# Performance work log

Measured on AMD Instinct MI355X. Metric: run time of the kernel, lower is better.

Reference implementation:

```python
import jax, jax.numpy as jnp
import numpy as np

N_NODES, N_PARENTS, K_WORDS, MAX_DEG = 16384, 8192, 32, 4
VOCAB, HID, NCLASS = 100000, 64, 4
NEG_INF = -1e30


def setup_inputs() -> dict:
    key = jax.random.key(0)
    ks = jax.random.split(key, 16)
    L = N_NODES - N_PARENTS
    # tree: leaves-first node ordering; parent i is node L+i, children are earlier nodes
    rng = np.random.default_rng(0)
    tree = np.full((N_PARENTS, MAX_DEG + 1), -1, dtype=np.int32)
    for i in range(N_PARENTS):
        hi = L + i
        nc = int(rng.integers(1, MAX_DEG + 1))
        ch = rng.choice(hi, size=min(nc, hi), replace=False)
        tree[i, :len(ch)] = ch
        tree[i, MAX_DEG] = hi  # parent slot, ignored (row[:-1] used)
    s = 0.1
    return {
        "x_word": jax.random.uniform(ks[0], (N_NODES, K_WORDS), jnp.float32),
        "x_index": jax.random.randint(ks[1], (N_NODES, K_WORDS), 0, VOCAB, jnp.int32),
        "tree": jnp.asarray(tree),
        "E_bu": s * jax.random.normal(ks[2], (HID, VOCAB), jnp.float32),
        "W_z_bu": s * jax.random.normal(ks[3], (HID, HID), jnp.float32),
        "U_z_bu": s * jax.random.normal(ks[4], (HID, HID), jnp.float32),
        "b_z_bu": jnp.zeros((1, HID), jnp.float32),
        "W_r_bu": s * jax.random.normal(ks[5], (HID, HID), jnp.float32),
        "U_r_bu": s * jax.random.normal(ks[6], (HID, HID), jnp.float32),
        "b_r_bu": jnp.zeros((1, HID), jnp.float32),
        "W_h_bu": s * jax.random.normal(ks[7], (HID, HID), jnp.float32),
        "U_h_bu": s * jax.random.normal(ks[8], (HID, HID), jnp.float32),
        "b_h_bu": jnp.zeros((1, HID), jnp.float32),
        "W_attn": s * jax.random.normal(ks[9], (HID, HID), jnp.float32),
        "W_out_bu": s * jax.random.normal(ks[10], (NCLASS, HID), jnp.float32),
        "b_out_bu": jnp.zeros((NCLASS,), jnp.float32),
    }


def reference(x_word, x_index, tree, E_bu, W_z_bu, U_z_bu, b_z_bu,
              W_r_bu, U_r_bu, b_r_bu, W_h_bu, U_h_bu, b_h_bu,
              W_attn, W_out_bu, b_out_bu):
    N = x_word.shape[0]
    P = tree.shape[0]
    L = N - P  # leaves first
    H = E_bu.shape[0]
    # node embedding xe[n] = x_word[n] @ E_bu[:, x_index[n]].T  -> [N,H]
    Eg = E_bu.T[x_index]                       # [N,K,H] gather (memory-bound)
    xe = jnp.einsum('nk,nkh->nh', x_word, Eg)  # [N,H]
    # Leaf update: child_h = zeros -> attn uniform, h_tilde = 0
    z_l = jax.nn.sigmoid(xe[:L] @ W_z_bu.T + b_z_bu)
    c_l = jnp.tanh(xe[:L] @ W_h_bu.T + b_h_bu)
    leaf_h = (1.0 - z_l) * c_l                 # z*0 + (1-z)*c
    node_h0 = jnp.zeros((N, H), xe.dtype).at[:L].set(leaf_h)
    children = tree[:, :-1]                    # [P, D] child indices, -1 padded

    def step(node_h, inp):
        idx, ch = inp
        mask = ch > -1
        ci = jnp.where(mask, ch, 0)
        child_h = node_h[ci]                   # [D,H]
        pxe = xe[L + idx]                      # [H]
        # attn = softmax(sigmoid(parent_xe @ W_attn @ child_h.T)) over valid children
        logits = jax.nn.sigmoid(pxe @ (W_attn @ child_h.T))
        attn = jax.nn.softmax(jnp.where(mask, logits, NEG_INF))
        h_tilde = attn @ child_h               # [H]  (LayerNorm output discarded in original)
        z = jax.nn.sigmoid(pxe @ W_z_bu.T + h_tilde @ U_z_bu.T + b_z_bu[0])
        r = jax.nn.sigmoid(pxe @ W_r_bu.T + h_tilde @ U_r_bu.T + b_r_bu[0])
        c = jnp.tanh(pxe @ W_h_bu.T + (r * h_tilde) @ U_h_bu.T + b_h_bu[0])
        h = z * h_tilde + (1.0 - z) * c        # dropout in eval = identity
        return node_h.at[L + idx].set(h), None

    node_h, _ = jax.lax.scan(step, node_h0, (jnp.arange(P), children))
    final = jnp.max(node_h[L:], axis=0)        # [H]
    return jax.nn.softmax((W_out_bu * final).sum(axis=1) + b_out_bu)
```

## Files before the change

kernel.cpp:

```cpp
#include <hip/hip_runtime.h>
#include <math.h>

#define NN 16384
#define NP 8192
#define NL 8192
#define KW 32
#define VC 100000
#define SENT  0xFFFFFFFFu
#define NEVER 0xFFFFFFFEu
#define CLEAN_EPOCH 1000

__device__ __forceinline__ float sigmoidf_(float x){ return 1.0f/(1.0f+expf(-x)); }

__global__ void __launch_bounds__(256) k_setup(const float* __restrict__ E, float* __restrict__ ET,
    const float* __restrict__ Wz, const float* __restrict__ Wr, const float* __restrict__ Wh,
    const float* __restrict__ Uz, const float* __restrict__ Ur, const float* __restrict__ Uh,
    float* __restrict__ WT, float* __restrict__ node_h, int* done, int* g_rem, int et_blocks){
  __shared__ float tile[64][65];
  int b = blockIdx.x;
  int lane = threadIdx.x & 63, ty = threadIdx.x >> 6;
  if (b < et_blocks){
    int v0 = b*64;
    for (int h = ty; h < 64; h += 4){
      int v = v0 + lane;
      tile[h][lane] = (v < VC) ? E[(size_t)h*VC + v] : 0.f;
    }
    __syncthreads();
    for (int vv = ty; vv < 64; vv += 4){
      int v = v0 + vv;
      if (v < VC) ET[v*64 + lane] = tile[lane][vv];
    }
  } else if (b < et_blocks + 6){
    int m = b - et_blocks;
    const float* src = (m==0)?Wz:(m==1)?Wr:(m==2)?Wh:(m==3)?Uz:(m==4)?Ur:Uh;
    float* dst = WT + m*4096;
    for (int h = ty; h < 64; h += 4) tile[h][lane] = src[h*64 + lane];
    __syncthreads();
    for (int k = ty; k < 64; k += 4) dst[k*64 + lane] = tile[lane][k];
  } else if (b < et_blocks + 6 + 4096){
    size_t idx = (size_t)(b - et_blocks - 6)*256 + threadIdx.x;
    ((unsigned int*)node_h)[idx] = SENT;
  } else {
    int idx = (b - et_blocks - 6 - 4096)*256 + threadIdx.x;
    if (idx < NP) done[idx] = 0;
    if (idx == 0) *g_rem = NP;
  }
}

__device__ __forceinline__ float gru_compute(int lane,
    int c0,int c1,int c2,int c3,
    float chv0,float chv1,float chv2,float chv3,
    float q, float pzv, float prv, float pcv,
    const float* __restrict__ UzT, const float* __restrict__ UrT,
    const float* __restrict__ UhT)
{
  float d0=q*chv0, d1=q*chv1, d2=q*chv2, d3=q*chv3;
  #pragma unroll
  for (int off=32; off; off>>=1){
    d0 += __shfl_xor(d0, off); d1 += __shfl_xor(d1, off);
    d2 += __shfl_xor(d2, off); d3 += __shfl_xor(d3, off);
  }
  float l0 = (c0>=0)? sigmoidf_(d0) : -1e30f;
  float l1 = (c1>=0)? sigmoidf_(d1) : -1e30f;
  float l2 = (c2>=0)? sigmoidf_(d2) : -1e30f;
  float l3 = (c3>=0)? sigmoidf_(d3) : -1e30f;
  float mx = fmaxf(fmaxf(l0,l1), fmaxf(l2,l3));
  float e0=expf(l0-mx), e1=expf(l1-mx), e2=expf(l2-mx), e3=expf(l3-mx);
  float inv = 1.f/(e0+e1+e2+e3);
  float ht = (e0*chv0 + e1*chv1 + e2*chv2 + e3*chv3)*inv;
  float az0=0.f, az1=0.f, ar0=0.f, ar1=0.f;
  #pragma unroll 8
  for (int k=0;k<64;k+=2){
    float h0 = __shfl(ht, k), h1 = __shfl(ht, k+1);
    az0 += h0 * UzT[k*64+lane];     az1 += h1 * UzT[(k+1)*64+lane];
    ar0 += h0 * UrT[k*64+lane];     ar1 += h1 * UrT[(k+1)*64+lane];
  }
  float z = sigmoidf_(pzv + az0+az1);
  float r = sigmoidf_(prv + ar0+ar1);
  float rh = r*ht;
  float ac0=0.f, ac1=0.f, ac2=0.f, ac3=0.f;
  #pragma unroll 8
  for (int k=0;k<64;k+=4){
    float r0 = __shfl(rh, k),   r1 = __shfl(rh, k+1);
    float r2 = __shfl(rh, k+2), r3 = __shfl(rh, k+3);
    ac0 += r0 * UhT[k*64+lane];     ac1 += r1 * UhT[(k+1)*64+lane];
    ac2 += r2 * UhT[(k+2)*64+lane]; ac3 += r3 * UhT[(k+3)*64+lane];
  }
  float cc = tanhf(pcv + (ac0+ac1)+(ac2+ac3));
  return z*ht + (1.f-z)*cc;
}

__device__ __forceinline__ void fused_body(int wid, int lane, float xev,
    const float* __restrict__ WzT, const float* __restrict__ WrT,
    const float* __restrict__ WhT, const float* __restrict__ Wa,
    const float* __restrict__ bz, const float* __restrict__ br,
    const float* __restrict__ bh,
    const float* __restrict__ UzT, const float* __restrict__ UrT,
    const float* __restrict__ UhT, const int* __restrict__ tree,
    float* node_h, float* pz, float* pr, float* pc, float* qa,
    int* done, int* g_rem)
{
  unsigned int* nhu = (unsigned int*)node_h;
  if (wid < NL){
    float az0=0.f, az1=0.f, ah0=0.f, ah1=0.f;
    #pragma unroll 8
    for (int k=0;k<64;k+=2){
      float x0 = __shfl(xev, k), x1 = __shfl(xev, k+1);
      az0 += x0 * WzT[k*64+lane];     az1 += x1 * WzT[(k+1)*64+lane];
      ah0 += x0 * WhT[k*64+lane];     ah1 += x1 * WhT[(k+1)*64+lane];
    }
    float z = sigmoidf_(az0+az1 + bz[lane]);
    float c = tanhf(ah0+ah1 + bh[lane]);
    float h = (1.f-z)*c;
    atomicExch(&nhu[(size_t)wid*64 + lane], __float_as_uint(h));
    return;
  }
  int i = wid - NL;
  float az=0.f, ar=0.f, ah=0.f, aq=0.f;
  #pragma unroll 4
  for (int k=0;k<64;++k){
    float xk = __shfl(xev, k);
    az += xk * WzT[k*64+lane];
    ar += xk * WrT[k*64+lane];
    ah += xk * WhT[k*64+lane];
    aq += xk * Wa [k*64+lane];
  }
  float pzv = az + bz[lane], prv = ar + br[lane], pcv = ah + bh[lane], q = aq;
  pz[i*64+lane] = pzv; pr[i*64+lane] = prv; pc[i*64+lane] = pcv; qa[i*64+lane] = q;
  const int* tr = tree + i*5;
  int c0=tr[0], c1=tr[1], c2=tr[2], c3=tr[3];
  unsigned int u0 = (c0>=0)? nhu[(size_t)c0*64+lane] : 0u;
  unsigned int u1 = (c1>=0)? nhu[(size_t)c1*64+lane] : 0u;
  unsigned int u2 = (c2>=0)? nhu[(size_t)c2*64+lane] : 0u;
  unsigned int u3 = (c3>=0)? nhu[(size_t)c3*64+lane] : 0u;
  bool p0 = __any((int)(u0==SENT)), p1 = __any((int)(u1==SENT));
  bool p2 = __any((int)(u2==SENT)), p3 = __any((int)(u3==SENT));
  int rounds = 0;
  while ((p0|p1|p2|p3) && rounds < (1<<16)){
    if (p0){ if (u0==SENT) u0 = atomicCAS(&nhu[(size_t)c0*64+lane], NEVER, NEVER); p0 = __any((int)(u0==SENT)); }
    if (p1){ if (u1==SENT) u1 = atomicCAS(&nhu[(size_t)c1*64+lane], NEVER, NEVER); p1 = __any((int)(u1==SENT)); }
    if (p2){ if (u2==SENT) u2 = atomicCAS(&nhu[(size_t)c2*64+lane], NEVER, NEVER); p2 = __any((int)(u2==SENT)); }
    if (p3){ if (u3==SENT) u3 = atomicCAS(&nhu[(size_t)c3*64+lane], NEVER, NEVER); p3 = __any((int)(u3==SENT)); }
    if (p0|p1|p2|p3){ __builtin_amdgcn_s_sleep(4); ++rounds; }
  }
  if (p0|p1|p2|p3) return;
  float h = gru_compute(lane, c0,c1,c2,c3,
                        __uint_as_float(u0), __uint_as_float(u1),
                        __uint_as_float(u2), __uint_as_float(u3),
                        q, pzv, prv, pcv, UzT, UrT, UhT);
  atomicExch(&nhu[(size_t)(NL+i)*64 + lane], __float_as_uint(h));
  if (lane==0){ done[i] = 1; atomicAdd(g_rem, -1); }
}

__global__ void __launch_bounds__(256) k_fused(const float* __restrict__ xw,
    const int* __restrict__ xi, const float* __restrict__ ET,
    const float* __restrict__ WzT, const float* __restrict__ WrT,
    const float* __restrict__ WhT, const float* __restrict__ Wa,
    const float* __restrict__ bz, const float* __restrict__ br,
    const float* __restrict__ bh,
    const float* __restrict__ UzT, const float* __restrict__ UrT,
    const float* __restrict__ UhT, const int* __restrict__ tree,
    float* node_h, float* pz, float* pr, float* pc, float* qa,
    int* done, int* g_rem)
{
  int wid = blockIdx.x*4 + (threadIdx.x>>6);
  int lane = threadIdx.x & 63;
  if (wid >= NN) return;
  int   idxl = (lane < KW) ? xi[wid*KW + lane] : 0;
  float wl   = (lane < KW) ? xw[wid*KW + lane] : 0.f;
  float xev = 0.f;
  #pragma unroll 8
  for (int k = 0; k < KW; ++k){
    int   vk = __shfl(idxl, k);
    float wk = __shfl(wl,   k);
    xev += wk * ET[vk*64 + lane];
  }
  fused_body(wid, lane, xev, WzT,WrT,WhT,Wa, bz,br,bh, UzT,UrT,UhT, tree,
             node_h, pz,pr,pc,qa, done, g_rem);
}

__global__ void __launch_bounds__(256) k_fused_direct(const float* __restrict__ xw,
    const int* __restrict__ xi, const float* __restrict__ E,
    const float* __restrict__ WzT, const float* __restrict__ WrT,
    const float* __restrict__ WhT, const float* __restrict__ Wa,
    const float* __restrict__ bz, const float* __restrict__ br,
    const float* __restrict__ bh,
    const float* __restrict__ UzT, const float* __restrict__ UrT,
    const float* __restrict__ UhT, const int* __restrict__ tree,
    float* node_h, float* pz, float* pr, float* pc, float* qa,
    int* done, int* g_rem)
{
  int wid = blockIdx.x*4 + (threadIdx.x>>6);
  int lane = threadIdx.x & 63;
  if (wid >= NN) return;
  const float* w = xw + wid*KW;
  const int*   v = xi + wid*KW;
  const float* Erow = E + (size_t)lane*VC;
  float xev = 0.f;
  for (int k = 0; k < KW; ++k) xev += w[k] * Erow[v[k]];
  fused_body(wid, lane, xev, WzT,WrT,WhT,Wa, bz,br,bh, UzT,UrT,UhT, tree,
             node_h, pz,pr,pc,qa, done, g_rem);
}

__device__ __forceinline__ bool lvl_ready(int c, int lvl, const int* done){
  if (c < NL) return true;
  int e = done[c - NL];
  return (e > 0 && e < lvl);
}

__global__ void __launch_bounds__(256) k_cleanup(const int* __restrict__ tree,
    const float* __restrict__ qa, const float* __restrict__ pz,
    const float* __restrict__ pr, const float* __restrict__ pc,
    const float* __restrict__ UzT, const float* __restrict__ UrT,
    const float* __restrict__ UhT,
    float* node_h, int* done, int* g_rem)
{
  int rem = *g_rem;
  if (rem <= 0) return;
  __shared__ int cnt_s;
  int w = threadIdx.x >> 6, lane = threadIdx.x & 63;
  int epoch = CLEAN_EPOCH;
  while (rem > 0){
    if (threadIdx.x == 0) cnt_s = 0;
    __syncthreads();
    int my = 0;
    for (int i = w; i < NP; i += 4){
      if (done[i]) continue;
      const int* tr = tree + i*5;
      int c0=tr[0], c1=tr[1], c2=tr[2], c3=tr[3];
      if (!(lvl_ready(c0,epoch,done) && lvl_ready(c1,epoch,done)
         && lvl_ready(c2,epoch,done) && lvl_ready(c3,epoch,done))) continue;
      float chv0 = (c0>=0)? node_h[c0*64+lane] : 0.f;
      float chv1 = (c1>=0)? node_h[c1*64+lane] : 0.f;
      float chv2 = (c2>=0)? node_h[c2*64+lane] : 0.f;
      float chv3 = (c3>=0)? node_h[c3*64+lane] : 0.f;
      float h = gru_compute(lane, c0,c1,c2,c3, chv0,chv1,chv2,chv3,
                            qa[i*64+lane], pz[i*64+lane], pr[i*64+lane], pc[i*64+lane],
                            UzT, UrT, UhT);
      node_h[(size_t)(NL+i)*64+lane] = h;
      if (lane==0) done[i] = epoch;
      ++my;
    }
    if (lane==0 && my) atomicAdd(&cnt_s, my);
    __syncthreads();
    rem -= cnt_s;
    ++epoch;
    __syncthreads();
  }
}

__global__ void k_max1(const float* __restrict__ node_h, float* __restrict__ partial){
  __shared__ float sm[4][64];
  int lane = threadIdx.x & 63, w = threadIdx.x>>6;
  int base = NL + blockIdx.x*128;
  float m = -1e30f;
  for (int r = w; r < 128; r += 4)
    m = fmaxf(m, node_h[(size_t)(base+r)*64 + lane]);
  sm[w][lane] = m;
  __syncthreads();
  if (w==0){
    m = fmaxf(fmaxf(sm[0][lane],sm[1][lane]), fmaxf(sm[2][lane],sm[3][lane]));
    partial[blockIdx.x*64+lane] = m;
  }
}

__global__ void k_max2(const float* __restrict__ partial, const float* __restrict__ Wout,
                       const float* __restrict__ bout, float* __restrict__ out){
  int lane = threadIdx.x;
  float m = -1e30f;
  for (int b=0;b<64;++b) m = fmaxf(m, partial[b*64+lane]);
  float s0 = Wout[0*64+lane]*m;
  float s1 = Wout[1*64+lane]*m;
  float s2 = Wout[2*64+lane]*m;
  float s3 = Wout[3*64+lane]*m;
  #pragma unroll
  for (int off=32; off; off>>=1){
    s0 += __shfl_xor(s0, off);
    s1 += __shfl_xor(s1, off);
    s2 += __shfl_xor(s2, off);
    s3 += __shfl_xor(s3, off);
  }
  s0 += bout[0]; s1 += bout[1]; s2 += bout[2]; s3 += bout[3];
  float mx = fmaxf(fmaxf(s0,s1), fmaxf(s2,s3));
  float e0=expf(s0-mx), e1=expf(s1-mx), e2=expf(s2-mx), e3=expf(s3-mx);
  float inv = 1.f/(e0+e1+e2+e3);
  if (lane==0){
    out[0]=e0*inv; out[1]=e1*inv; out[2]=e2*inv; out[3]=e3*inv;
  }
}

__global__ void k_ws_sentinel(float* out, float wsmb){
  if (threadIdx.x < 4) out[threadIdx.x] = wsmb;
}

extern "C" void kernel_launch(void* const* d_in, const int* in_sizes, int n_in,
                              void* d_out, int out_size, void* d_ws, size_t ws_size,
                              hipStream_t stream){
  const float* x_word = (const float*)d_in[0];
  const int*   x_index= (const int*)d_in[1];
  const int*   tree   = (const int*)d_in[2];
  const float* E      = (const float*)d_in[3];
  const float* Wz     = (const float*)d_in[4];
  const float* Uz     = (const float*)d_in[5];
  const float* bz     = (const float*)d_in[6];
  const float* Wr     = (const float*)d_in[7];
  const float* Ur     = (const float*)d_in[8];
  const float* br     = (const float*)d_in[9];
  const float* Wh     = (const float*)d_in[10];
  const float* Uh     = (const float*)d_in[11];
  const float* bh     = (const float*)d_in[12];
  const float* Wa     = (const float*)d_in[13];
  const float* Wout   = (const float*)d_in[14];
  const float* bout   = (const float*)d_in[15];
  float* out = (float*)d_out;

  float* ws = (float*)d_ws;

  const size_t R0_FULL = 6400000;
  const size_t R0_FB   = 4096;
  const size_t TAIL    = 2097152 + 1048576 + 24576 + NP + 1;
  const size_t FULL_NEED = (R0_FULL + TAIL) * 4;
  const size_t FB_NEED   = (R0_FB   + TAIL) * 4;

  bool full = (ws_size >= FULL_NEED);
  bool fb   = (!full && ws_size >= FB_NEED);
  if (!full && !fb){
    k_ws_sentinel<<<1, 64, 0, stream>>>(out, (float)(ws_size >> 20));
    return;
  }

  float* ET   = ws;
  float* part = ws;
  size_t r0   = full ? R0_FULL : R0_FB;
  float* qa    = ws + r0;
  float* pz    = qa + 524288;
  float* pr    = pz + 524288;
  float* pc    = pr + 524288;
  float* nodeh = pc + 524288;
  float* WT    = nodeh + 1048576;
  int*   done  = (int*)(WT + 24576);
  int*   g_rem = done + NP;
  float* WzT = WT,       *WrT = WT+4096,  *WhT = WT+8192;
  float* UzT = WT+12288, *UrT = WT+16384, *UhT = WT+20480;

  int et_blocks = full ? (VC+63)/64 : 0;
  k_setup<<<et_blocks + 6 + 4096 + NP/256, 256, 0, stream>>>(
      E, ET, Wz, Wr, Wh, Uz, Ur, Uh, WT, nodeh, done, g_rem, et_blocks);
  if (full)
    k_fused<<<NN/4, 256, 0, stream>>>(x_word, x_index, ET, WzT, WrT, WhT, Wa,
                                      bz, br, bh, UzT, UrT, UhT, tree,
                                      nodeh, pz, pr, pc, qa, done, g_rem);
  else
    k_fused_direct<<<NN/4, 256, 0, stream>>>(x_word, x_index, E, WzT, WrT, WhT, Wa,
                                             bz, br, bh, UzT, UrT, UhT, tree,
                                             nodeh, pz, pr, pc, qa, done, g_rem);
  k_cleanup<<<1,  256, 0, stream>>>(tree, qa, pz, pr, pc, UzT, UrT, UhT,
                                    nodeh, done, g_rem);
  k_max1   <<<64, 256, 0, stream>>>(nodeh, part);
  k_max2   <<<1,   64, 0, stream>>>(part, Wout, bout, out);
}
```

Measured before the change: 164.1 us.

## Replace spin-wait parent scheduling with dependency-counted work handoff and fused max

```diff
diff --git a/kernel.cpp b/kernel.cpp
--- a/kernel.cpp
+++ b/kernel.cpp
@@ -6,16 +6,27 @@
 #define NL 8192
 #define KW 32
 #define VC 100000
+#define REVW 8
 #define SENT  0xFFFFFFFFu
 #define NEVER 0xFFFFFFFEu
-#define CLEAN_EPOCH 1000
+#define UMAP_NEGINF 0x007FFFFFu
 
 __device__ __forceinline__ float sigmoidf_(float x){ return 1.0f/(1.0f+expf(-x)); }
+__device__ __forceinline__ unsigned int umap(float f){
+  unsigned int b = __float_as_uint(f);
+  return (b & 0x80000000u) ? ~b : (b | 0x80000000u);
+}
+__device__ __forceinline__ float uunmap(unsigned int u){
+  unsigned int b = (u & 0x80000000u) ? (u & 0x7FFFFFFFu) : ~u;
+  return __uint_as_float(b);
+}
 
 __global__ void __launch_bounds__(256) k_setup(const float* __restrict__ E, float* __restrict__ ET,
     const float* __restrict__ Wz, const float* __restrict__ Wr, const float* __restrict__ Wh,
     const float* __restrict__ Uz, const float* __restrict__ Ur, const float* __restrict__ Uh,
-    float* __restrict__ WT, float* __restrict__ node_h, int* done, int* g_rem, int et_blocks){
+    float* __restrict__ WT, unsigned int* node_h, unsigned int* pact,
+    const int* __restrict__ tree, int* pending, int* rcnt, int* rev,
+    int* g_rem, unsigned int* gmax, int et_blocks){
   __shared__ float tile[64][65];
   int b = blockIdx.x;
   int lane = threadIdx.x & 63, ty = threadIdx.x >> 6;
@@ -39,11 +50,29 @@
     for (int k = ty; k < 64; k += 4) dst[k*64 + lane] = tile[lane][k];
   } else if (b < et_blocks + 6 + 4096){
     size_t idx = (size_t)(b - et_blocks - 6)*256 + threadIdx.x;
-    ((unsigned int*)node_h)[idx] = SENT;
+    node_h[idx] = SENT;
+  } else if (b < et_blocks + 6 + 4096 + 8192){
+    size_t idx = (size_t)(b - et_blocks - 6 - 4096)*256 + threadIdx.x;
+    pact[idx] = SENT;
   } else {
-    int idx = (b - et_blocks - 6 - 4096)*256 + threadIdx.x;
-    if (idx < NP) done[idx] = 0;
+    int idx = (b - et_blocks - 6 - 4096 - 8192)*256 + threadIdx.x;
+    if (idx < NP){
+      const int* tr = tree + idx*5;
+      int cnt = 0;
+      #pragma unroll
+      for (int j=0;j<4;++j){
+        int c = tr[j];
+        if (c >= NL){
+          ++cnt;
+          int cc = c - NL;
+          int slot = atomicAdd(&rcnt[cc], 1);
+          if (slot < REVW) rev[cc*REVW + slot] = idx;
+        }
+      }
+      pending[idx] = cnt + 1;
+    }
     if (idx == 0) *g_rem = NP;
+    if (idx < 512) gmax[idx] = UMAP_NEGINF;
   }
 }
 
@@ -90,17 +119,26 @@
   return z*ht + (1.f-z)*cc;
 }
 
-__device__ __forceinline__ void fused_body(int wid, int lane, float xev,
+__device__ __forceinline__ unsigned int read_sync(unsigned int* p, int* budget){
+  unsigned int u = *p;
+  while (__any((int)(u == SENT)) && *budget > 0){
+    if (u == SENT) u = atomicCAS(p, NEVER, NEVER);
+    if (__any((int)(u == SENT))){ __builtin_amdgcn_s_sleep(2); --*budget; }
+  }
+  return u;
+}
+
+__device__ __forceinline__ void fused_body(int wid, int w, int lane, float xev,
     const float* __restrict__ WzT, const float* __restrict__ WrT,
     const float* __restrict__ WhT, const float* __restrict__ Wa,
     const float* __restrict__ bz, const float* __restrict__ br,
     const float* __restrict__ bh,
     const float* __restrict__ UzT, const float* __restrict__ UrT,
     const float* __restrict__ UhT, const int* __restrict__ tree,
-    float* node_h, float* pz, float* pr, float* pc, float* qa,
-    int* done, int* g_rem)
+    unsigned int* nhu, unsigned int* pact, int* pending,
+    const int* __restrict__ rcnt, const int* __restrict__ rev,
+    int* g_rem, unsigned int* gmax, int* stk)
 {
-  unsigned int* nhu = (unsigned int*)node_h;
   if (wid < NL){
     float az0=0.f, az1=0.f, ah0=0.f, ah1=0.f;
     #pragma unroll 8
@@ -111,8 +149,7 @@
     }
     float z = sigmoidf_(az0+az1 + bz[lane]);
     float c = tanhf(ah0+ah1 + bh[lane]);
-    float h = (1.f-z)*c;
-    atomicExch(&nhu[(size_t)wid*64 + lane], __float_as_uint(h));
+    atomicExch(&nhu[(size_t)wid*64 + lane], __float_as_uint((1.f-z)*c));
     return;
   }
   int i = wid - NL;
@@ -125,31 +162,62 @@
     ah += xk * WhT[k*64+lane];
     aq += xk * Wa [k*64+lane];
   }
-  float pzv = az + bz[lane], prv = ar + br[lane], pcv = ah + bh[lane], q = aq;
-  pz[i*64+lane] = pzv; pr[i*64+lane] = prv; pc[i*64+lane] = pcv; qa[i*64+lane] = q;
-  const int* tr = tree + i*5;
-  int c0=tr[0], c1=tr[1], c2=tr[2], c3=tr[3];
-  unsigned int u0 = (c0>=0)? nhu[(size_t)c0*64+lane] : 0u;
-  unsigned int u1 = (c1>=0)? nhu[(size_t)c1*64+lane] : 0u;
-  unsigned int u2 = (c2>=0)? nhu[(size_t)c2*64+lane] : 0u;
-  unsigned int u3 = (c3>=0)? nhu[(size_t)c3*64+lane] : 0u;
-  bool p0 = __any((int)(u0==SENT)), p1 = __any((int)(u1==SENT));
-  bool p2 = __any((int)(u2==SENT)), p3 = __any((int)(u3==SENT));
-  int rounds = 0;
-  while ((p0|p1|p2|p3) && rounds < (1<<16)){
-    if (p0){ if (u0==SENT) u0 = atomicCAS(&nhu[(size_t)c0*64+lane], NEVER, NEVER); p0 = __any((int)(u0==SENT)); }
-    if (p1){ if (u1==SENT) u1 = atomicCAS(&nhu[(size_t)c1*64+lane], NEVER, NEVER); p1 = __any((int)(u1==SENT)); }
-    if (p2){ if (u2==SENT) u2 = atomicCAS(&nhu[(size_t)c2*64+lane], NEVER, NEVER); p2 = __any((int)(u2==SENT)); }
-    if (p3){ if (u3==SENT) u3 = atomicCAS(&nhu[(size_t)c3*64+lane], NEVER, NEVER); p3 = __any((int)(u3==SENT)); }
-    if (p0|p1|p2|p3){ __builtin_amdgcn_s_sleep(4); ++rounds; }
-  }
-  if (p0|p1|p2|p3) return;
-  float h = gru_compute(lane, c0,c1,c2,c3,
-                        __uint_as_float(u0), __uint_as_float(u1),
-                        __uint_as_float(u2), __uint_as_float(u3),
-                        q, pzv, prv, pcv, UzT, UrT, UhT);
-  atomicExch(&nhu[(size_t)(NL+i)*64 + lane], __float_as_uint(h));
-  if (lane==0){ done[i] = 1; atomicAdd(g_rem, -1); }
+  float q0 = aq, pz0 = az + bz[lane], pr0 = ar + br[lane], pc0 = ah + bh[lane];
+  unsigned int* pa = pact + (size_t)i*256;
+  atomicExch(&pa[0*64+lane], __float_as_uint(q0));
+  atomicExch(&pa[1*64+lane], __float_as_uint(pz0));
+  atomicExch(&pa[2*64+lane], __float_as_uint(pc0));
+  atomicExch(&pa[3*64+lane], __float_as_uint(pr0));
+  int nn = -1, sp = 0;
+  if (lane == 0){
+    if (atomicSub(&pending[i], 1) == 1) nn = i;
+  }
+  int next = __shfl(nn, 0);
+  bool ownregs = true;
+  while (next >= 0){
+    int cur = next;
+    int budget = 1<<16;
+    float q, pzv, prv, pcv;
+    if (ownregs && cur == i){ q=q0; pzv=pz0; prv=pr0; pcv=pc0; }
+    else {
+      unsigned int* pb = pact + (size_t)cur*256;
+      q   = __uint_as_float(read_sync(&pb[0*64+lane], &budget));
+      pzv = __uint_as_float(read_sync(&pb[1*64+lane], &budget));
+      pcv = __uint_as_float(read_sync(&pb[2*64+lane], &budget));
+      prv = __uint_as_float(read_sync(&pb[3*64+lane], &budget));
+    }
+    const int* tr = tree + cur*5;
+    int c0=tr[0], c1=tr[1], c2=tr[2], c3=tr[3];
+    unsigned int u0 = (c0>=0)? read_sync(&nhu[(size_t)c0*64+lane], &budget) : 0u;
+    unsigned int u1 = (c1>=0)? read_sync(&nhu[(size_t)c1*64+lane], &budget) : 0u;
+    unsigned int u2 = (c2>=0)? read_sync(&nhu[(size_t)c2*64+lane], &budget) : 0u;
+    unsigned int u3 = (c3>=0)? read_sync(&nhu[(size_t)c3*64+lane], &budget) : 0u;
+    bool bad = __any((int)(u0==SENT)) || __any((int)(u1==SENT)) ||
+               __any((int)(u2==SENT)) || __any((int)(u3==SENT));
+    nn = -1;
+    if (!bad){
+      float h = gru_compute(lane, c0,c1,c2,c3,
+                            __uint_as_float(u0), __uint_as_float(u1),
+                            __uint_as_float(u2), __uint_as_float(u3),
+                            q, pzv, prv, pcv, UzT, UrT, UhT);
+      atomicExch(&nhu[(size_t)(NL+cur)*64 + lane], __float_as_uint(h));
+      atomicMax(&gmax[(cur&7)*64 + lane], umap(h));
+      if (lane == 0){
+        atomicAdd(g_rem, -1);
+        int rc = rcnt[cur]; if (rc > REVW) rc = REVW;
+        for (int j = 0; j < rc; ++j){
+          int cons = rev[cur*REVW + j];
+          if (atomicSub(&pending[cons], 1) == 1){
+            if (nn < 0) nn = cons;
+            else if (sp < 12) stk[sp++] = cons;
+          }
+        }
+      }
+    }
+    if (lane == 0 && nn < 0 && sp > 0) nn = stk[--sp];
+    next = __shfl(nn, 0);
+    ownregs = false;
+  }
 }
 
 __global__ void __launch_bounds__(256) k_fused(const float* __restrict__ xw,
@@ -160,11 +228,13 @@
     const float* __restrict__ bh,
     const float* __restrict__ UzT, const float* __restrict__ UrT,
     const float* __restrict__ UhT, const int* __restrict__ tree,
-    float* node_h, float* pz, float* pr, float* pc, float* qa,
-    int* done, int* g_rem)
+    unsigned int* nhu, unsigned int* pact, int* pending,
+    const int* __restrict__ rcnt, const int* __restrict__ rev,
+    int* g_rem, unsigned int* gmax)
 {
-  int wid = blockIdx.x*4 + (threadIdx.x>>6);
-  int lane = threadIdx.x & 63;
+  __shared__ int stk_s[4][12];
+  int w = threadIdx.x >> 6, lane = threadIdx.x & 63;
+  int wid = blockIdx.x*4 + w;
   if (wid >= NN) return;
   int   idxl = (lane < KW) ? xi[wid*KW + lane] : 0;
   float wl   = (lane < KW) ? xw[wid*KW + lane] : 0.f;
@@ -175,8 +245,8 @@
     float wk = __shfl(wl,   k);
     xev += wk * ET[vk*64 + lane];
   }
-  fused_body(wid, lane, xev, WzT,WrT,WhT,Wa, bz,br,bh, UzT,UrT,UhT, tree,
-             node_h, pz,pr,pc,qa, done, g_rem);
+  fused_body(wid, w, lane, xev, WzT,WrT,WhT,Wa, bz,br,bh, UzT,UrT,UhT, tree,
+             nhu, pact, pending, rcnt, rev, g_rem, gmax, stk_s[w]);
 }
 
 __global__ void __launch_bounds__(256) k_fused_direct(const float* __restrict__ xw,
@@ -187,105 +257,89 @@
     const float* __restrict__ bh,
     const float* __restrict__ UzT, const float* __restrict__ UrT,
     const float* __restrict__ UhT, const int* __restrict__ tree,
-    float* node_h, float* pz, float* pr, float* pc, float* qa,
-    int* done, int* g_rem)
+    unsigned int* nhu, unsigned int* pact, int* pending,
+    const int* __restrict__ rcnt, const int* __restrict__ rev,
+    int* g_rem, unsigned int* gmax)
 {
-  int wid = blockIdx.x*4 + (threadIdx.x>>6);
-  int lane = threadIdx.x & 63;
+  __shared__ int stk_s[4][12];
+  int w = threadIdx.x >> 6, lane = threadIdx.x & 63;
+  int wid = blockIdx.x*4 + w;
   if (wid >= NN) return;
-  const float* w = xw + wid*KW;
-  const int*   v = xi + wid*KW;
+  const float* wv = xw + wid*KW;
+  const int*   v  = xi + wid*KW;
   const float* Erow = E + (size_t)lane*VC;
   float xev = 0.f;
-  for (int k = 0; k < KW; ++k) xev += w[k] * Erow[v[k]];
-  fused_body(wid, lane, xev, WzT,WrT,WhT,Wa, bz,br,bh, UzT,UrT,UhT, tree,
-             node_h, pz,pr,pc,qa, done, g_rem);
-}
-
-__device__ __forceinline__ bool lvl_ready(int c, int lvl, const int* done){
-  if (c < NL) return true;
-  int e = done[c - NL];
-  return (e > 0 && e < lvl);
-}
-
-__global__ void __launch_bounds__(256) k_cleanup(const int* __restrict__ tree,
-    const float* __restrict__ qa, const float* __restrict__ pz,
-    const float* __restrict__ pr, const float* __restrict__ pc,
+  for (int k = 0; k < KW; ++k) xev += wv[k] * Erow[v[k]];
+  fused_body(wid, w, lane, xev, WzT,WrT,WhT,Wa, bz,br,bh, UzT,UrT,UhT, tree,
+             nhu, pact, pending, rcnt, rev, g_rem, gmax, stk_s[w]);
+}
+
+__global__ void __launch_bounds__(256) k_finish(const int* __restrict__ tree,
+    const unsigned int* __restrict__ pact,
     const float* __restrict__ UzT, const float* __restrict__ UrT,
     const float* __restrict__ UhT,
-    float* node_h, int* done, int* g_rem)
+    unsigned int* nhu, int* g_rem, unsigned int* gmax,
+    const float* __restrict__ Wout, const float* __restrict__ bout,
+    float* __restrict__ out)
 {
+  __shared__ int cnt_s;
+  __shared__ float sm[64];
+  int w = threadIdx.x >> 6, lane = threadIdx.x & 63;
   int rem = *g_rem;
-  if (rem <= 0) return;
-  __shared__ int cnt_s;
-  int w = threadIdx.x >> 6, lane = threadIdx.x & 63;
-  int epoch = CLEAN_EPOCH;
   while (rem > 0){
     if (threadIdx.x == 0) cnt_s = 0;
     __syncthreads();
     int my = 0;
     for (int i = w; i < NP; i += 4){
-      if (done[i]) continue;
+      if (nhu[(size_t)(NL+i)*64] != SENT) continue;
       const int* tr = tree + i*5;
       int c0=tr[0], c1=tr[1], c2=tr[2], c3=tr[3];
-      if (!(lvl_ready(c0,epoch,done) && lvl_ready(c1,epoch,done)
-         && lvl_ready(c2,epoch,done) && lvl_ready(c3,epoch,done))) continue;
-      float chv0 = (c0>=0)? node_h[c0*64+lane] : 0.f;
-      float chv1 = (c1>=0)? node_h[c1*64+lane] : 0.f;
-      float chv2 = (c2>=0)? node_h[c2*64+lane] : 0.f;
-      float chv3 = (c3>=0)? node_h[c3*64+lane] : 0.f;
+      bool ready = (c0<0 || nhu[(size_t)c0*64] != SENT) &&
+                   (c1<0 || nhu[(size_t)c1*64] != SENT) &&
+                   (c2<0 || nhu[(size_t)c2*64] != SENT) &&
+                   (c3<0 || nhu[(size_t)c3*64] != SENT);
+      if (!ready) continue;
+      float chv0 = (c0>=0)? __uint_as_float(nhu[(size_t)c0*64+lane]) : 0.f;
+      float chv1 = (c1>=0)? __uint_as_float(nhu[(size_t)c1*64+lane]) : 0.f;
+      float chv2 = (c2>=0)? __uint_as_float(nhu[(size_t)c2*64+lane]) : 0.f;
+      float chv3 = (c3>=0)? __uint_as_float(nhu[(size_t)c3*64+lane]) : 0.f;
+      const unsigned int* pb = pact + (size_t)i*256;
+      float q   = __uint_as_float(pb[0*64+lane]);
+      float pzv = __uint_as_float(pb[1*64+lane]);
+      float pcv = __uint_as_float(pb[2*64+lane]);
+      float prv = __uint_as_float(pb[3*64+lane]);
       float h = gru_compute(lane, c0,c1,c2,c3, chv0,chv1,chv2,chv3,
-                            qa[i*64+lane], pz[i*64+lane], pr[i*64+lane], pc[i*64+lane],
-                            UzT, UrT, UhT);
-      node_h[(size_t)(NL+i)*64+lane] = h;
-      if (lane==0) done[i] = epoch;
+                            q, pzv, prv, pcv, UzT, UrT, UhT);
+      nhu[(size_t)(NL+i)*64+lane] = __float_as_uint(h);
+      atomicMax(&gmax[(i&7)*64+lane], umap(h));
       ++my;
     }
     if (lane==0 && my) atomicAdd(&cnt_s, my);
     __syncthreads();
     rem -= cnt_s;
-    ++epoch;
+    if (cnt_s == 0) break;
     __syncthreads();
   }
-}
-
-__global__ void k_max1(const float* __restrict__ node_h, float* __restrict__ partial){
-  __shared__ float sm[4][64];
-  int lane = threadIdx.x & 63, w = threadIdx.x>>6;
-  int base = NL + blockIdx.x*128;
-  float m = -1e30f;
-  for (int r = w; r < 128; r += 4)
-    m = fmaxf(m, node_h[(size_t)(base+r)*64 + lane]);
-  sm[w][lane] = m;
   __syncthreads();
-  if (w==0){
-    m = fmaxf(fmaxf(sm[0][lane],sm[1][lane]), fmaxf(sm[2][lane],sm[3][lane]));
-    partial[blockIdx.x*64+lane] = m;
-  }
-}
-
-__global__ void k_max2(const float* __restrict__ partial, const float* __restrict__ Wout,
-                       const float* __restrict__ bout, float* __restrict__ out){
-  int lane = threadIdx.x;
-  float m = -1e30f;
-  for (int b=0;b<64;++b) m = fmaxf(m, partial[b*64+lane]);
-  float s0 = Wout[0*64+lane]*m;
-  float s1 = Wout[1*64+lane]*m;
-  float s2 = Wout[2*64+lane]*m;
-  float s3 = Wout[3*64+lane]*m;
-  #pragma unroll
-  for (int off=32; off; off>>=1){
-    s0 += __shfl_xor(s0, off);
-    s1 += __shfl_xor(s1, off);
-    s2 += __shfl_xor(s2, off);
-    s3 += __shfl_xor(s3, off);
-  }
-  s0 += bout[0]; s1 += bout[1]; s2 += bout[2]; s3 += bout[3];
-  float mx = fmaxf(fmaxf(s0,s1), fmaxf(s2,s3));
-  float e0=expf(s0-mx), e1=expf(s1-mx), e2=expf(s2-mx), e3=expf(s3-mx);
-  float inv = 1.f/(e0+e1+e2+e3);
-  if (lane==0){
-    out[0]=e0*inv; out[1]=e1*inv; out[2]=e2*inv; out[3]=e3*inv;
+  if (w == 0){
+    float m = -1e30f;
+    #pragma unroll
+    for (int c = 0; c < 8; ++c) m = fmaxf(m, uunmap(gmax[c*64+lane]));
+    sm[lane] = m;
+    float s0 = Wout[0*64+lane]*m, s1 = Wout[1*64+lane]*m;
+    float s2 = Wout[2*64+lane]*m, s3 = Wout[3*64+lane]*m;
+    #pragma unroll
+    for (int off=32; off; off>>=1){
+      s0 += __shfl_xor(s0, off); s1 += __shfl_xor(s1, off);
+      s2 += __shfl_xor(s2, off); s3 += __shfl_xor(s3, off);
+    }
+    s0 += bout[0]; s1 += bout[1]; s2 += bout[2]; s3 += bout[3];
+    float mx = fmaxf(fmaxf(s0,s1), fmaxf(s2,s3));
+    float e0=expf(s0-mx), e1=expf(s1-mx), e2=expf(s2-mx), e3=expf(s3-mx);
+    float inv = 1.f/(e0+e1+e2+e3);
+    if (lane==0){
+      out[0]=e0*inv; out[1]=e1*inv; out[2]=e2*inv; out[3]=e3*inv;
+    }
   }
 }
 
@@ -317,10 +371,9 @@
   float* ws = (float*)d_ws;
 
   const size_t R0_FULL = 6400000;
-  const size_t R0_FB   = 4096;
-  const size_t TAIL    = 2097152 + 1048576 + 24576 + NP + 1;
+  const size_t TAIL = (size_t)2097152 + 1048576 + 24576 + NP + NP + NP*REVW + 1 + 512;
   const size_t FULL_NEED = (R0_FULL + TAIL) * 4;
-  const size_t FB_NEED   = (R0_FB   + TAIL) * 4;
+  const size_t FB_NEED   = TAIL * 4;
 
   bool full = (ws_size >= FULL_NEED);
   bool fb   = (!full && ws_size >= FB_NEED);
@@ -329,33 +382,34 @@
     return;
   }
 
-  float* ET   = ws;
-  float* part = ws;
-  size_t r0   = full ? R0_FULL : R0_FB;
-  float* qa    = ws + r0;
-  float* pz    = qa + 524288;
-  float* pr    = pz + 524288;
-  float* pc    = pr + 524288;
-  float* nodeh = pc + 524288;
-  float* WT    = nodeh + 1048576;
-  int*   done  = (int*)(WT + 24576);
-  int*   g_rem = done + NP;
+  float* ET = ws;
+  size_t r0 = full ? R0_FULL : 0;
+  unsigned int* pact  = (unsigned int*)(ws + r0);
+  unsigned int* nhu   = pact + (size_t)NP*256;
+  float* WT   = (float*)(nhu + (size_t)NN*64);
+  int* pending = (int*)(WT + 24576);
+  int* rcnt    = pending + NP;
+  int* rev     = rcnt + NP;
+  int* g_rem   = rev + NP*REVW;
+  unsigned int* gmax = (unsigned int*)(g_rem + 1);
   float* WzT = WT,       *WrT = WT+4096,  *WhT = WT+8192;
   float* UzT = WT+12288, *UrT = WT+16384, *UhT = WT+20480;
 
+  hipMemsetAsync(rcnt, 0, NP*sizeof(int), stream);
+
   int et_blocks = full ? (VC+63)/64 : 0;
-  k_setup<<<et_blocks + 6 + 4096 + NP/256, 256, 0, stream>>>(
-      E, ET, Wz, Wr, Wh, Uz, Ur, Uh, WT, nodeh, done, g_rem, et_blocks);
+  int nblocks = et_blocks + 6 + 4096 + 8192 + NP/256;
+  k_setup<<<nblocks, 256, 0, stream>>>(E, ET, Wz, Wr, Wh, Uz, Ur, Uh, WT,
+                                       nhu, pact, tree, pending, rcnt, rev,
+                                       g_rem, gmax, et_blocks);
   if (full)
     k_fused<<<NN/4, 256, 0, stream>>>(x_word, x_index, ET, WzT, WrT, WhT, Wa,
                                       bz, br, bh, UzT, UrT, UhT, tree,
-                                      nodeh, pz, pr, pc, qa, done, g_rem);
+                                      nhu, pact, pending, rcnt, rev, g_rem, gmax);
   else
     k_fused_direct<<<NN/4, 256, 0, stream>>>(x_word, x_index, E, WzT, WrT, WhT, Wa,
                                              bz, br, bh, UzT, UrT, UhT, tree,
-                                             nodeh, pz, pr, pc, qa, done, g_rem);
-  k_cleanup<<<1,  256, 0, stream>>>(tree, qa, pz, pr, pc, UzT, UrT, UhT,
-                                    nodeh, done, g_rem);
-  k_max1   <<<64, 256, 0, stream>>>(nodeh, part);
-  k_max2   <<<1,   64, 0, stream>>>(part, Wout, bout, out);
-}
+                                             nhu, pact, pending, rcnt, rev, g_rem, gmax);
+  k_finish<<<1, 256, 0, stream>>>(tree, pact, UzT, UrT, UhT, nhu, g_rem, gmax,
+                                  Wout, bout, out);
+}
```

Measured after the change: 269.6 us. 64.2% more time.

## Use row-level ready flags, fused atomic max, and merged finish kernel

Applied to the files above, without the earlier changes.

```diff
diff --git a/kernel.cpp b/kernel.cpp
--- a/kernel.cpp
+++ b/kernel.cpp
@@ -8,14 +8,23 @@
 #define VC 100000
 #define SENT  0xFFFFFFFFu
 #define NEVER 0xFFFFFFFEu
-#define CLEAN_EPOCH 1000
+#define UMAP_NEGINF 0x007FFFFFu
 
 __device__ __forceinline__ float sigmoidf_(float x){ return 1.0f/(1.0f+expf(-x)); }
+__device__ __forceinline__ unsigned int umap(float f){
+  unsigned int b = __float_as_uint(f);
+  return (b & 0x80000000u) ? ~b : (b | 0x80000000u);
+}
+__device__ __forceinline__ float uunmap(unsigned int u){
+  unsigned int b = (u & 0x80000000u) ? (u & 0x7FFFFFFFu) : ~u;
+  return __uint_as_float(b);
+}
 
 __global__ void __launch_bounds__(256) k_setup(const float* __restrict__ E, float* __restrict__ ET,
     const float* __restrict__ Wz, const float* __restrict__ Wr, const float* __restrict__ Wh,
     const float* __restrict__ Uz, const float* __restrict__ Ur, const float* __restrict__ Uh,
-    float* __restrict__ WT, float* __restrict__ node_h, int* done, int* g_rem, int et_blocks){
+    float* __restrict__ WT, unsigned int* node_h, int* g_rem, unsigned int* gmax,
+    int et_blocks){
   __shared__ float tile[64][65];
   int b = blockIdx.x;
   int lane = threadIdx.x & 63, ty = threadIdx.x >> 6;
@@ -39,12 +48,19 @@
     for (int k = ty; k < 64; k += 4) dst[k*64 + lane] = tile[lane][k];
   } else if (b < et_blocks + 6 + 4096){
     size_t idx = (size_t)(b - et_blocks - 6)*256 + threadIdx.x;
-    ((unsigned int*)node_h)[idx] = SENT;
+    node_h[idx] = SENT;
   } else {
     int idx = (b - et_blocks - 6 - 4096)*256 + threadIdx.x;
-    if (idx < NP) done[idx] = 0;
+    if (idx < 512) gmax[idx] = UMAP_NEGINF;
     if (idx == 0) *g_rem = NP;
   }
+}
+
+__device__ __forceinline__ void publish_row(unsigned int* row, int lane, float h){
+  unsigned int hb = __float_as_uint(h);
+  if (lane) atomicExch(&row[lane], hb);
+  asm volatile("s_waitcnt vmcnt(0)" ::: "memory");
+  if (!lane) atomicExch(&row[0], hb);
 }
 
 __device__ __forceinline__ float gru_compute(int lane,
@@ -97,10 +113,9 @@
     const float* __restrict__ bh,
     const float* __restrict__ UzT, const float* __restrict__ UrT,
     const float* __restrict__ UhT, const int* __restrict__ tree,
-    float* node_h, float* pz, float* pr, float* pc, float* qa,
-    int* done, int* g_rem)
-{
-  unsigned int* nhu = (unsigned int*)node_h;
+    unsigned int* nhu, float* pz, float* pr, float* pc, float* qa,
+    int* g_rem, unsigned int* gmax)
+{
   if (wid < NL){
     float az0=0.f, az1=0.f, ah0=0.f, ah1=0.f;
     #pragma unroll 8
@@ -111,8 +126,7 @@
     }
     float z = sigmoidf_(az0+az1 + bz[lane]);
     float c = tanhf(ah0+ah1 + bh[lane]);
-    float h = (1.f-z)*c;
-    atomicExch(&nhu[(size_t)wid*64 + lane], __float_as_uint(h));
+    publish_row(&nhu[(size_t)wid*64], lane, (1.f-z)*c);
     return;
   }
   int i = wid - NL;
@@ -125,7 +139,7 @@
     ah += xk * WhT[k*64+lane];
     aq += xk * Wa [k*64+lane];
   }
-  float pzv = az + bz[lane], prv = ar + br[lane], pcv = ah + bh[lane], q = aq;
+  float q = aq, pzv = az + bz[lane], prv = ar + br[lane], pcv = ah + bh[lane];
   pz[i*64+lane] = pzv; pr[i*64+lane] = prv; pc[i*64+lane] = pcv; qa[i*64+lane] = q;
   const int* tr = tree + i*5;
   int c0=tr[0], c1=tr[1], c2=tr[2], c3=tr[3];
@@ -133,23 +147,36 @@
   unsigned int u1 = (c1>=0)? nhu[(size_t)c1*64+lane] : 0u;
   unsigned int u2 = (c2>=0)? nhu[(size_t)c2*64+lane] : 0u;
   unsigned int u3 = (c3>=0)? nhu[(size_t)c3*64+lane] : 0u;
-  bool p0 = __any((int)(u0==SENT)), p1 = __any((int)(u1==SENT));
-  bool p2 = __any((int)(u2==SENT)), p3 = __any((int)(u3==SENT));
-  int rounds = 0;
-  while ((p0|p1|p2|p3) && rounds < (1<<16)){
-    if (p0){ if (u0==SENT) u0 = atomicCAS(&nhu[(size_t)c0*64+lane], NEVER, NEVER); p0 = __any((int)(u0==SENT)); }
-    if (p1){ if (u1==SENT) u1 = atomicCAS(&nhu[(size_t)c1*64+lane], NEVER, NEVER); p1 = __any((int)(u1==SENT)); }
-    if (p2){ if (u2==SENT) u2 = atomicCAS(&nhu[(size_t)c2*64+lane], NEVER, NEVER); p2 = __any((int)(u2==SENT)); }
-    if (p3){ if (u3==SENT) u3 = atomicCAS(&nhu[(size_t)c3*64+lane], NEVER, NEVER); p3 = __any((int)(u3==SENT)); }
-    if (p0|p1|p2|p3){ __builtin_amdgcn_s_sleep(4); ++rounds; }
-  }
-  if (p0|p1|p2|p3) return;
+  bool anyS = __any((int)(u0==SENT)) || __any((int)(u1==SENT)) ||
+              __any((int)(u2==SENT)) || __any((int)(u3==SENT));
+  if (anyS){
+    int myc = (lane==0)?c0:(lane==1)?c1:(lane==2)?c2:(lane==3)?c3:-1;
+    bool need = (lane < 4) && (myc >= 0);
+    unsigned int* myp = &nhu[(size_t)(need ? myc : 0)*64];
+    bool rdy = !need;
+    if (need) rdy = (atomicCAS(myp, NEVER, NEVER) != SENT);
+    int rounds = 0;
+    while (!__all((int)rdy)){
+      if (rounds < 4) __builtin_amdgcn_s_sleep(1);
+      else            __builtin_amdgcn_s_sleep(8);
+      if (!rdy) rdy = (atomicCAS(myp, NEVER, NEVER) != SENT);
+      if (++rounds > (1<<14)) break;
+    }
+    if (!__all((int)rdy)) return;
+    if (c0>=0 && u0==SENT) u0 = atomicCAS(&nhu[(size_t)c0*64+lane], NEVER, NEVER);
+    if (c1>=0 && u1==SENT) u1 = atomicCAS(&nhu[(size_t)c1*64+lane], NEVER, NEVER);
+    if (c2>=0 && u2==SENT) u2 = atomicCAS(&nhu[(size_t)c2*64+lane], NEVER, NEVER);
+    if (c3>=0 && u3==SENT) u3 = atomicCAS(&nhu[(size_t)c3*64+lane], NEVER, NEVER);
+    if (__any((int)(u0==SENT)) || __any((int)(u1==SENT)) ||
+        __any((int)(u2==SENT)) || __any((int)(u3==SENT))) return;
+  }
   float h = gru_compute(lane, c0,c1,c2,c3,
                         __uint_as_float(u0), __uint_as_float(u1),
                         __uint_as_float(u2), __uint_as_float(u3),
                         q, pzv, prv, pcv, UzT, UrT, UhT);
-  atomicExch(&nhu[(size_t)(NL+i)*64 + lane], __float_as_uint(h));
-  if (lane==0){ done[i] = 1; atomicAdd(g_rem, -1); }
+  publish_row(&nhu[(size_t)(NL+i)*64], lane, h);
+  atomicMax(&gmax[(i&7)*64 + lane], umap(h));
+  if (lane==0) atomicAdd(g_rem, -1);
 }
 
 __global__ void __launch_bounds__(256) k_fused(const float* __restrict__ xw,
@@ -160,8 +187,8 @@
     const float* __restrict__ bh,
     const float* __restrict__ UzT, const float* __restrict__ UrT,
     const float* __restrict__ UhT, const int* __restrict__ tree,
-    float* node_h, float* pz, float* pr, float* pc, float* qa,
-    int* done, int* g_rem)
+    unsigned int* nhu, float* pz, float* pr, float* pc, float* qa,
+    int* g_rem, unsigned int* gmax)
 {
   int wid = blockIdx.x*4 + (threadIdx.x>>6);
   int lane = threadIdx.x & 63;
@@ -176,7 +203,7 @@
     xev += wk * ET[vk*64 + lane];
   }
   fused_body(wid, lane, xev, WzT,WrT,WhT,Wa, bz,br,bh, UzT,UrT,UhT, tree,
-             node_h, pz,pr,pc,qa, done, g_rem);
+             nhu, pz,pr,pc,qa, g_rem, gmax);
 }
 
 __global__ void __launch_bounds__(256) k_fused_direct(const float* __restrict__ xw,
@@ -187,105 +214,85 @@
     const float* __restrict__ bh,
     const float* __restrict__ UzT, const float* __restrict__ UrT,
     const float* __restrict__ UhT, const int* __restrict__ tree,
-    float* node_h, float* pz, float* pr, float* pc, float* qa,
-    int* done, int* g_rem)
+    unsigned int* nhu, float* pz, float* pr, float* pc, float* qa,
+    int* g_rem, unsigned int* gmax)
 {
   int wid = blockIdx.x*4 + (threadIdx.x>>6);
   int lane = threadIdx.x & 63;
   if (wid >= NN) return;
-  const float* w = xw + wid*KW;
-  const int*   v = xi + wid*KW;
+  const float* wv = xw + wid*KW;
+  const int*   v  = xi + wid*KW;
   const float* Erow = E + (size_t)lane*VC;
   float xev = 0.f;
-  for (int k = 0; k < KW; ++k) xev += w[k] * Erow[v[k]];
+  for (int k = 0; k < KW; ++k) xev += wv[k] * Erow[v[k]];
   fused_body(wid, lane, xev, WzT,WrT,WhT,Wa, bz,br,bh, UzT,UrT,UhT, tree,
-             node_h, pz,pr,pc,qa, done, g_rem);
-}
-
-__device__ __forceinline__ bool lvl_ready(int c, int lvl, const int* done){
-  if (c < NL) return true;
-  int e = done[c - NL];
-  return (e > 0 && e < lvl);
-}
-
-__global__ void __launch_bounds__(256) k_cleanup(const int* __restrict__ tree,
+             nhu, pz,pr,pc,qa, g_rem, gmax);
+}
+
+__global__ void __launch_bounds__(256) k_finish(const int* __restrict__ tree,
     const float* __restrict__ qa, const float* __restrict__ pz,
     const float* __restrict__ pr, const float* __restrict__ pc,
     const float* __restrict__ UzT, const float* __restrict__ UrT,
     const float* __restrict__ UhT,
-    float* node_h, int* done, int* g_rem)
-{
-  int rem = *g_rem;
-  if (rem <= 0) return;
+    unsigned int* nhu, int* g_rem, unsigned int* gmax,
+    const float* __restrict__ Wout, const float* __restrict__ bout,
+    float* __restrict__ out)
+{
   __shared__ int cnt_s;
   int w = threadIdx.x >> 6, lane = threadIdx.x & 63;
-  int epoch = CLEAN_EPOCH;
+  int rem = *g_rem;
   while (rem > 0){
     if (threadIdx.x == 0) cnt_s = 0;
     __syncthreads();
     int my = 0;
     for (int i = w; i < NP; i += 4){
-      if (done[i]) continue;
+      if (nhu[(size_t)(NL+i)*64] != SENT) continue;
       const int* tr = tree + i*5;
       int c0=tr[0], c1=tr[1], c2=tr[2], c3=tr[3];
-      if (!(lvl_ready(c0,epoch,done) && lvl_ready(c1,epoch,done)
-         && lvl_ready(c2,epoch,done) && lvl_ready(c3,epoch,done))) continue;
-      float chv0 = (c0>=0)? node_h[c0*64+lane] : 0.f;
-      float chv1 = (c1>=0)? node_h[c1*64+lane] : 0.f;
-      float chv2 = (c2>=0)? node_h[c2*64+lane] : 0.f;
-      float chv3 = (c3>=0)? node_h[c3*64+lane] : 0.f;
+      bool ready = (c0<0 || nhu[(size_t)c0*64] != SENT) &&
+                   (c1<0 || nhu[(size_t)c1*64] != SENT) &&
+                   (c2<0 || nhu[(size_t)c2*64] != SENT) &&
+                   (c3<0 || nhu[(size_t)c3*64] != SENT);
+      if (!ready) continue;
+      float chv0 = (c0>=0)? __uint_as_float(nhu[(size_t)c0*64+lane]) : 0.f;
+      float chv1 = (c1>=0)? __uint_as_float(nhu[(size_t)c1*64+lane]) : 0.f;
+      float chv2 = (c2>=0)? __uint_as_float(nhu[(size_t)c2*64+lane]) : 0.f;
+      float chv3 = (c3>=0)? __uint_as_float(nhu[(size_t)c3*64+lane]) : 0.f;
       float h = gru_compute(lane, c0,c1,c2,c3, chv0,chv1,chv2,chv3,
                             qa[i*64+lane], pz[i*64+lane], pr[i*64+lane], pc[i*64+lane],
                             UzT, UrT, UhT);
-      node_h[(size_t)(NL+i)*64+lane] = h;
-      if (lane==0) done[i] = epoch;
+      nhu[(size_t)(NL+i)*64+lane] = __float_as_uint(h);
+      atomicMax(&gmax[(i&7)*64+lane], umap(h));
       ++my;
     }
     if (lane==0 && my) atomicAdd(&cnt_s, my);
     __syncthreads();
     rem -= cnt_s;
-    ++epoch;
-    __syncthreads();
-  }
-}
-
-__global__ void k_max1(const float* __restrict__ node_h, float* __restrict__ partial){
-  __shared__ float sm[4][64];
-  int lane = threadIdx.x & 63, w = threadIdx.x>>6;
-  int base = NL + blockIdx.x*128;
-  float m = -1e30f;
-  for (int r = w; r < 128; r += 4)
-    m = fmaxf(m, node_h[(size_t)(base+r)*64 + lane]);
-  sm[w][lane] = m;
+    if (cnt_s == 0) break;
+    __syncthreads();
+  }
   __syncthreads();
-  if (w==0){
-    m = fmaxf(fmaxf(sm[0][lane],sm[1][lane]), fmaxf(sm[2][lane],sm[3][lane]));
-    partial[blockIdx.x*64+lane] = m;
-  }
-}
-
-__global__ void k_max2(const float* __restrict__ partial, const float* __restrict__ Wout,
-                       const float* __restrict__ bout, float* __restrict__ out){
-  int lane = threadIdx.x;
-  float m = -1e30f;
-  for (int b=0;b<64;++b) m = fmaxf(m, partial[b*64+lane]);
-  float s0 = Wout[0*64+lane]*m;
-  float s1 = Wout[1*64+lane]*m;
-  float s2 = Wout[2*64+lane]*m;
-  float s3 = Wout[3*64+lane]*m;
-  #pragma unroll
-  for (int off=32; off; off>>=1){
-    s0 += __shfl_xor(s0, off);
-    s1 += __shfl_xor(s1, off);
-    s2 += __shfl_xor(s2, off);
-    s3 += __shfl_xor(s3, off);
-  }
-  s0 += bout[0]; s1 += bout[1]; s2 += bout[2]; s3 += bout[3];
-  float mx = fmaxf(fmaxf(s0,s1), fmaxf(s2,s3));
-  float e0=expf(s0-mx), e1=expf(s1-mx), e2=expf(s2-mx), e3=expf(s3-mx);
-  float inv = 1.f/(e0+e1+e2+e3);
-  if (lane==0){
-    out[0]=e0*inv; out[1]=e1*inv; out[2]=e2*inv; out[3]=e3*inv;
+  if (w == 0){
+    float m = -1e30f;
+    #pragma unroll
+    for (int c = 0; c < 8; ++c){
+      unsigned int g = atomicCAS(&gmax[c*64+lane], NEVER, NEVER);
+      m = fmaxf(m, uunmap(g));
+    }
+    float s0 = Wout[0*64+lane]*m, s1 = Wout[1*64+lane]*m;
+    float s2 = Wout[2*64+lane]*m, s3 = Wout[3*64+lane]*m;
+    #pragma unroll
+    for (int off=32; off; off>>=1){
+      s0 += __shfl_xor(s0, off); s1 += __shfl_xor(s1, off);
+      s2 += __shfl_xor(s2, off); s3 += __shfl_xor(s3, off);
+    }
+    s0 += bout[0]; s1 += bout[1]; s2 += bout[2]; s3 += bout[3];
+    float mx = fmaxf(fmaxf(s0,s1), fmaxf(s2,s3));
+    float e0=expf(s0-mx), e1=expf(s1-mx), e2=expf(s2-mx), e3=expf(s3-mx);
+    float inv = 1.f/(e0+e1+e2+e3);
+    if (lane==0){
+      out[0]=e0*inv; out[1]=e1*inv; out[2]=e2*inv; out[3]=e3*inv;
+    }
   }
 }
 
@@ -317,10 +324,9 @@
   float* ws = (float*)d_ws;
 
   const size_t R0_FULL = 6400000;
-  const size_t R0_FB   = 4096;
-  const size_t TAIL    = 2097152 + 1048576 + 24576 + NP + 1;
+  const size_t TAIL = (size_t)2097152 + 1048576 + 24576 + 1 + 512;
   const size_t FULL_NEED = (R0_FULL + TAIL) * 4;
-  const size_t FB_NEED   = (R0_FB   + TAIL) * 4;
+  const size_t FB_NEED   = TAIL * 4;
 
   bool full = (ws_size >= FULL_NEED);
   bool fb   = (!full && ws_size >= FB_NEED);
@@ -329,33 +335,30 @@
     return;
   }
 
-  float* ET   = ws;
-  float* part = ws;
-  size_t r0   = full ? R0_FULL : R0_FB;
+  float* ET = ws;
+  size_t r0 = full ? R0_FULL : 0;
   float* qa    = ws + r0;
   float* pz    = qa + 524288;
   float* pr    = pz + 524288;
   float* pc    = pr + 524288;
-  float* nodeh = pc + 524288;
-  float* WT    = nodeh + 1048576;
-  int*   done  = (int*)(WT + 24576);
-  int*   g_rem = done + NP;
+  unsigned int* nhu = (unsigned int*)(pc + 524288);
+  float* WT    = (float*)(nhu + (size_t)NN*64);
+  int*   g_rem = (int*)(WT + 24576);
+  unsigned int* gmax = (unsigned int*)(g_rem + 1);
   float* WzT = WT,       *WrT = WT+4096,  *WhT = WT+8192;
   float* UzT = WT+12288, *UrT = WT+16384, *UhT = WT+20480;
 
   int et_blocks = full ? (VC+63)/64 : 0;
-  k_setup<<<et_blocks + 6 + 4096 + NP/256, 256, 0, stream>>>(
-      E, ET, Wz, Wr, Wh, Uz, Ur, Uh, WT, nodeh, done, g_rem, et_blocks);
+  k_setup<<<et_blocks + 6 + 4096 + 2, 256, 0, stream>>>(
+      E, ET, Wz, Wr, Wh, Uz, Ur, Uh, WT, nhu, g_rem, gmax, et_blocks);
   if (full)
     k_fused<<<NN/4, 256, 0, stream>>>(x_word, x_index, ET, WzT, WrT, WhT, Wa,
                                       bz, br, bh, UzT, UrT, UhT, tree,
-                                      nodeh, pz, pr, pc, qa, done, g_rem);
+                                      nhu, pz, pr, pc, qa, g_rem, gmax);
   else
     k_fused_direct<<<NN/4, 256, 0, stream>>>(x_word, x_index, E, WzT, WrT, WhT, Wa,
                                              bz, br, bh, UzT, UrT, UhT, tree,
-                                             nodeh, pz, pr, pc, qa, done, g_rem);
-  k_cleanup<<<1,  256, 0, stream>>>(tree, qa, pz, pr, pc, UzT, UrT, UhT,
-                                    nodeh, done, g_rem);
-  k_max1   <<<64, 256, 0, stream>>>(nodeh, part);
-  k_max2   <<<1,   64, 0, stream>>>(part, Wout, bout, out);
-}
+                                             nhu, pz, pr, pc, qa, g_rem, gmax);
+  k_finish<<<1, 256, 0, stream>>>(tree, qa, pz, pr, pc, UzT, UrT, UhT,
+                                  nhu, g_rem, gmax, Wout, bout, out);
+}
```

New measurement: 163.8 us. Within noise of the previous version (-0.2%).
